# Optimization experiments

Hardware: AMD Instinct MI355X
Metric: run time of the kernel (lower is better)

## Reference

```python
import jax, jax.numpy as jnp
import numpy as np

B, N, E = 2, 20000, 160000
D, U = 1, 100          # input_dim, num_units
IN = D + U             # 101
NEG_SLOPE = 0.2        # PyG GATv2Conv default


def setup_inputs() -> dict:
    key = jax.random.key(0)
    ks = jax.random.split(key, 20)
    s = 0.1
    inp = {
        "inputs": jax.random.normal(ks[0], (B, N * D), jnp.float32),
        "state": jax.random.normal(ks[1], (B, N * U), jnp.float32),
        "src": jax.random.randint(ks[2], (E,), 0, N),
        "dst": jax.random.randint(ks[3], (E,), 0, N),
        # GATv2Conv(101, 200) params: lin_l, lin_r, att, out-bias
        "Wl1": jax.random.normal(ks[4], (IN, 2 * U), jnp.float32) * s,
        "bl1": jax.random.normal(ks[5], (2 * U,), jnp.float32) * s,
        "Wr1": jax.random.normal(ks[6], (IN, 2 * U), jnp.float32) * s,
        "br1": jax.random.normal(ks[7], (2 * U,), jnp.float32) * s,
        "att1": jax.random.normal(ks[8], (2 * U,), jnp.float32) * s,
        "bg1": jax.random.normal(ks[9], (2 * U,), jnp.float32) * s,
        "bias0": jax.random.normal(ks[10], (2 * U,), jnp.float32) * s,
        # GATv2Conv(101, 100) params
        "Wl2": jax.random.normal(ks[11], (IN, U), jnp.float32) * s,
        "bl2": jax.random.normal(ks[12], (U,), jnp.float32) * s,
        "Wr2": jax.random.normal(ks[13], (IN, U), jnp.float32) * s,
        "br2": jax.random.normal(ks[14], (U,), jnp.float32) * s,
        "att2": jax.random.normal(ks[15], (U,), jnp.float32) * s,
        "bg2": jax.random.normal(ks[16], (U,), jnp.float32) * s,
        "bias1": jax.random.normal(ks[17], (U,), jnp.float32) * s,
    }
    return inp


def _gatv2(x, src_f, dst_f, Wl, bl, Wr, br, att, bg):
    # x: (B, N, IN); edges (with self-loops) flow src -> dst.
    xl = x @ Wl + bl                                   # (B, N, C) source transform
    xr = x @ Wr + br                                   # (B, N, C) target transform
    msg = jax.nn.leaky_relu(xl[:, src_f] + xr[:, dst_f], NEG_SLOPE)  # (B, Ef, C)
    e = jnp.einsum('bec,c->be', msg, att)              # (B, Ef) attention logits
    seg_max = jax.vmap(lambda v: jax.ops.segment_max(v, dst_f, num_segments=N))(e)
    ea = jnp.exp(e - seg_max[:, dst_f])
    denom = jax.vmap(lambda v: jax.ops.segment_sum(v, dst_f, num_segments=N))(ea)
    alpha = ea / denom[:, dst_f]                       # per-target softmax
    out = jax.vmap(
        lambda a, xs: jax.ops.segment_sum(a[:, None] * xs, dst_f, num_segments=N)
    )(alpha, xl[:, src_f])                             # (B, N, C)
    return out + bg


def reference(inputs, state, src, dst,
              Wl1, bl1, Wr1, br1, att1, bg1, bias0,
              Wl2, bl2, Wr2, br2, att2, bg2, bias1):
    loops = jnp.arange(N)
    src_f = jnp.concatenate([src, loops])              # PyG adds self-loops
    dst_f = jnp.concatenate([dst, loops])
    inputs3 = inputs.reshape(B, N, D)
    state3 = state.reshape(B, N, U)

    # _gc1: GATv2(101 -> 200) + bias_0, sigmoid gates r, u
    xs = jnp.concatenate([inputs3, state3], axis=2)    # (B, N, 101)
    g1 = _gatv2(xs, src_f, dst_f, Wl1, bl1, Wr1, br1, att1, bg1) + bias0
    val = jax.nn.sigmoid(g1)                           # (B, N, 200)
    r = val[..., :U].reshape(B, N * U)
    u = val[..., U:].reshape(B, N * U)

    # _gc2: GATv2(101 -> 100) on [inputs, r*state] + bias_1, tanh
    xs2 = jnp.concatenate([inputs3, (r * state).reshape(B, N, U)], axis=2)
    c = jnp.tanh(_gatv2(xs2, src_f, dst_f, Wl2, bl2, Wr2, br2, att2, bg2) + bias1)
    c = c.reshape(B, N * U)

    new_state = u * state + (1.0 - u) * c              # (B, N*U)
    return new_state
```

## Files before the change

### kernel.cpp

```cpp
#include <hip/hip_runtime.h>
#include <stdint.h>

typedef __attribute__((ext_vector_type(8))) short short8;
typedef __attribute__((ext_vector_type(4))) short short4v;
typedef __attribute__((ext_vector_type(4))) float f32x4;

static constexpr int BB = 2, NN = 20000, UU = 100;
static constexpr int C1 = 200, C2 = 100;
static constexpr int MT = BB * NN;
static constexpr int MPAD = 40064;
static constexpr float NEG = 0.2f;

__device__ __forceinline__ float b2f(short s) {
  union { uint32_t u; float f; } cv; cv.u = ((uint32_t)(uint16_t)s) << 16; return cv.f;
}
__device__ __forceinline__ short f2b(float x) {
  union { float f; uint32_t u; } cv; cv.f = x;
  uint32_t r = cv.u + 0x7FFFu + ((cv.u >> 16) & 1u);
  return (short)(r >> 16);
}

#define GL2LDS(gsrc, ldst)                                                          \
  __builtin_amdgcn_global_load_lds((const __attribute__((address_space(1))) void*)(gsrc), \
                                   (__attribute__((address_space(3))) void*)(ldst), 16, 0, 0)


__global__ void k_prep(const float* __restrict__ inp, const float* __restrict__ st,
                       const float* __restrict__ Wl1, const float* __restrict__ Wr1,
                       const float* __restrict__ Wl2, const float* __restrict__ Wr2,
                       short* __restrict__ A, short* __restrict__ BT1,
                       short* __restrict__ BT2, int* __restrict__ cursor) {
  int t = blockIdx.x * 256 + threadIdx.x;
  if (t < MT * 16) {
    int r = t >> 4, g = t & 15;
    short8 v;
#pragma unroll
    for (int j = 0; j < 8; ++j) {
      int e = g * 8 + j;
      float x = 0.f;
      if (e == 0) x = inp[r];
      else if (e <= 100) x = st[(size_t)r * 100 + e - 1];
      v[j] = f2b(x);
    }
    *(short8*)(A + (size_t)r * 128 + ((g ^ (r & 7)) << 3)) = v;
  }
  if (t < 512 * 16) {
    int n = t >> 4, g = t & 15;
    short8 v;
#pragma unroll
    for (int j = 0; j < 8; ++j) {
      int k = g * 8 + j;
      float x = 0.f;
      if (k < 101 && n < 400)
        x = (n < 200) ? Wl1[(size_t)k * 200 + n] : Wr1[(size_t)k * 200 + n - 200];
      v[j] = f2b(x);
    }
    *(short8*)(BT1 + (size_t)n * 128 + ((g ^ (n & 7)) << 3)) = v;
  }
  if (t < 256 * 16) {
    int n = t >> 4, g = t & 15;
    short8 v;
#pragma unroll
    for (int j = 0; j < 8; ++j) {
      int k = g * 8 + j;
      int ksrc = (k < 100) ? k + 1 : ((k == 100) ? 0 : -1);
      float x = 0.f;
      if (ksrc >= 0 && n < 200)
        x = (n < 100) ? Wl2[(size_t)ksrc * 100 + n] : Wr2[(size_t)ksrc * 100 + n - 100];
      v[j] = f2b(x);
    }
    *(short8*)(BT2 + (size_t)n * 128 + ((g ^ (n & 7)) << 3)) = v;
  }
  if (t < NN) cursor[t] = 0;
}


__global__ void k_hist(const int* __restrict__ dst, int E, int* __restrict__ hist) {
  int e = blockIdx.x * 256 + threadIdx.x;
  if (e < E) atomicAdd(&hist[dst[e]], 1);
}

__global__ __launch_bounds__(1024) void k_scan(int* __restrict__ histcur,
                                               int* __restrict__ rowptr, int N, int E) {
  __shared__ int part[1024];
  int t = threadIdx.x;
  int CH = (N + 1023) / 1024;
  int beg = t * CH; if (beg > N) beg = N;
  int end = beg + CH; if (end > N) end = N;
  int s = 0;
  for (int i = beg; i < end; ++i) s += histcur[i];
  part[t] = s;
  __syncthreads();
  for (int off = 1; off < 1024; off <<= 1) {
    int v = (t >= off) ? part[t - off] : 0;
    __syncthreads();
    part[t] += v;
    __syncthreads();
  }
  int base = (t == 0) ? 0 : part[t - 1];
  for (int i = beg; i < end; ++i) {
    int h = histcur[i];
    rowptr[i] = base;
    histcur[i] = base;
    base += h;
  }
  if (t == 1023) rowptr[N] = part[1023];
}

__global__ void k_scatter(const int* __restrict__ src, const int* __restrict__ dst, int E,
                          int* __restrict__ cursor, int* __restrict__ col) {
  int e = blockIdx.x * 256 + threadIdx.x;
  if (e < E) {
    int p = atomicAdd(&cursor[dst[e]], 1);
    col[p] = src[e];
  }
}


template<int NOUT, int SPLIT>
__global__ __launch_bounds__(256) void k_gemm(
    const short* __restrict__ A, const short* __restrict__ BT,
    const float* __restrict__ bias_l, const float* __restrict__ bias_r,
    short* __restrict__ X) {
  __shared__ __align__(16) short As[128 * 128];
  __shared__ __align__(16) short Bs[128 * 128];
  int tid = threadIdx.x;
  int m0 = blockIdx.x * 128;
  int n0 = blockIdx.y * 128;
  {
    const short* gA = A + (size_t)m0 * 128;
    const short* gB = BT + (size_t)n0 * 128;
#pragma unroll
    for (int i = 0; i < 8; ++i) {
      GL2LDS(gA + i * 2048 + tid * 8, As + i * 2048 + tid * 8);
      GL2LDS(gB + i * 2048 + tid * 8, Bs + i * 2048 + tid * 8);
    }
  }
  __syncthreads();

  int wv = tid >> 6, lane = tid & 63;
  int m_off = (wv & 1) * 64, n_off = (wv >> 1) * 64;
  int lrow = lane & 15, lk = lane >> 4;
  f32x4 acc[4][4];
#pragma unroll
  for (int i = 0; i < 4; ++i)
#pragma unroll
    for (int j = 0; j < 4; ++j) acc[i][j] = (f32x4){0.f, 0.f, 0.f, 0.f};

#pragma unroll
  for (int kk = 0; kk < 4; ++kk) {
    int g = kk * 4 + lk;
    short8 a[4], b[4];
#pragma unroll
    for (int f = 0; f < 4; ++f) {
      int ra = m_off + f * 16 + lrow;
      a[f] = *(const short8*)(As + ra * 128 + ((g ^ (ra & 7)) << 3));
      int rb = n_off + f * 16 + lrow;
      b[f] = *(const short8*)(Bs + rb * 128 + ((g ^ (rb & 7)) << 3));
    }
#pragma unroll
    for (int i = 0; i < 4; ++i)
#pragma unroll
      for (int j = 0; j < 4; ++j)
        acc[i][j] = __builtin_amdgcn_mfma_f32_16x16x32_bf16(a[i], b[j], acc[i][j], 0, 0, 0);
  }

#pragma unroll
  for (int j = 0; j < 4; ++j) {
    int nc = n0 + n_off + j * 16 + lrow;
    bool nok = nc < NOUT;
    float bv = 0.f;
    int coff = 0;
    if (nok) {
      bv   = (nc < SPLIT) ? bias_l[nc] : bias_r[nc - SPLIT];
      coff = (nc < SPLIT) ? nc : 2 * SPLIT + (nc - SPLIT);
    }
#pragma unroll
    for (int i = 0; i < 4; ++i) {
      int mb = m0 + m_off + i * 16 + lk * 4;
#pragma unroll
      for (int r = 0; r < 4; ++r) {
        int m = mb + r;
        if (nok && m < MT) {
          int b_   = (m >= NN) ? 1 : 0;
          int node = m - b_ * NN;
          X[(size_t)node * (4 * SPLIT) + coff + b_ * SPLIT] = f2b(acc[i][j][r] + bv);
        }
      }
    }
  }
}


__global__ __launch_bounds__(256) void k_agg1(
    const short* __restrict__ X1, const int* __restrict__ rowptr, const int* __restrict__ col,
    const float* __restrict__ att, const float* __restrict__ bgv, const float* __restrict__ bias0,
    const float* __restrict__ st, const float* __restrict__ inp,
    short* __restrict__ A2, float* __restrict__ uu) {
  int w = threadIdx.x >> 6, lane = threadIdx.x & 63;
  int n = blockIdx.x * 4 + w;
  if (n >= NN) return;
  int half = lane >> 5, ll = lane & 31;
  int c0 = (ll < 25 ? ll : 24) * 8;
  int idx = half * NN + n;
  const short* xb = X1 + (size_t)half * 200 + c0;

  float attv[8], xrv[8], num[8];
  {
    f32x4 a0 = (f32x4){0,0,0,0}, a1 = (f32x4){0,0,0,0};
    if (ll < 25) { a0 = *(const f32x4*)(att + c0); a1 = *(const f32x4*)(att + c0 + 4); }
#pragma unroll
    for (int q = 0; q < 4; ++q) { attv[q] = a0[q]; attv[4 + q] = a1[q]; }
    short8 xr8 = *(const short8*)(X1 + (size_t)n * 800 + 400 + half * 200 + c0);
#pragma unroll
    for (int q = 0; q < 8; ++q) xrv[q] = (ll < 25) ? b2f(xr8[q]) : 0.f;
  }
  float denom;
  {
    short8 v = *(const short8*)(xb + (size_t)n * 800);
    float xs[8], e = 0.f;
#pragma unroll
    for (int q = 0; q < 8; ++q) {
      xs[q] = b2f(v[q]);
      float msg = xs[q] + xrv[q];
      msg = (msg > 0.f) ? msg : NEG * msg;
      e = fmaf(msg, attv[q], e);
    }
#pragma unroll
    for (int off = 16; off > 0; off >>= 1) e += __shfl_xor(e, off);
    float pe = __expf(e);
    denom = pe;
#pragma unroll
    for (int q = 0; q < 8; ++q) num[q] = pe * xs[q];
  }

  int beg = rowptr[n], end = rowptr[n + 1];
  for (int bp = beg; bp < end; bp += 64) {
    int cnt = min(end - bp, 64);
    int cv = col[bp + (lane < cnt ? lane : 0)];
    int p = 0;
    for (; p + 4 <= cnt; p += 4) {
      int s0 = __shfl(cv, p), s1 = __shfl(cv, p + 1);
      int s2 = __shfl(cv, p + 2), s3 = __shfl(cv, p + 3);
      short8 v0 = *(const short8*)(xb + (size_t)s0 * 800);
      short8 v1 = *(const short8*)(xb + (size_t)s1 * 800);
      short8 v2 = *(const short8*)(xb + (size_t)s2 * 800);
      short8 v3 = *(const short8*)(xb + (size_t)s3 * 800);
      float xs0[8], xs1[8], xs2[8], xs3[8];
      float e0 = 0.f, e1 = 0.f, e2 = 0.f, e3 = 0.f;
#pragma unroll
      for (int q = 0; q < 8; ++q) {
        float m_;
        xs0[q] = b2f(v0[q]); m_ = xs0[q] + xrv[q]; m_ = (m_ > 0.f) ? m_ : NEG * m_; e0 = fmaf(m_, attv[q], e0);
        xs1[q] = b2f(v1[q]); m_ = xs1[q] + xrv[q]; m_ = (m_ > 0.f) ? m_ : NEG * m_; e1 = fmaf(m_, attv[q], e1);
        xs2[q] = b2f(v2[q]); m_ = xs2[q] + xrv[q]; m_ = (m_ > 0.f) ? m_ : NEG * m_; e2 = fmaf(m_, attv[q], e2);
        xs3[q] = b2f(v3[q]); m_ = xs3[q] + xrv[q]; m_ = (m_ > 0.f) ? m_ : NEG * m_; e3 = fmaf(m_, attv[q], e3);
      }
#pragma unroll
      for (int off = 16; off > 0; off >>= 1) {
        e0 += __shfl_xor(e0, off);
        e1 += __shfl_xor(e1, off);
        e2 += __shfl_xor(e2, off);
        e3 += __shfl_xor(e3, off);
      }
      float pe0 = __expf(e0), pe1 = __expf(e1), pe2 = __expf(e2), pe3 = __expf(e3);
      denom += (pe0 + pe1) + (pe2 + pe3);
#pragma unroll
      for (int q = 0; q < 8; ++q)
        num[q] = fmaf(pe3, xs3[q], fmaf(pe2, xs2[q], fmaf(pe1, xs1[q], fmaf(pe0, xs0[q], num[q]))));
    }
    for (; p < cnt; ++p) {
      int s0 = __shfl(cv, p);
      short8 v0 = *(const short8*)(xb + (size_t)s0 * 800);
      float xs0[8], e0 = 0.f;
#pragma unroll
      for (int q = 0; q < 8; ++q) {
        xs0[q] = b2f(v0[q]);
        float m_ = xs0[q] + xrv[q]; m_ = (m_ > 0.f) ? m_ : NEG * m_;
        e0 = fmaf(m_, attv[q], e0);
      }
#pragma unroll
      for (int off = 16; off > 0; off >>= 1) e0 += __shfl_xor(e0, off);
      float pe0 = __expf(e0);
      denom += pe0;
#pragma unroll
      for (int q = 0; q < 8; ++q) num[q] = fmaf(pe0, xs0[q], num[q]);
    }
  }

  float invd = 1.f / denom;
  if (ll < 25) {
    f32x4 g0 = *(const f32x4*)(bgv + c0),   g1 = *(const f32x4*)(bgv + c0 + 4);
    f32x4 h0 = *(const f32x4*)(bias0 + c0), h1 = *(const f32x4*)(bias0 + c0 + 4);
    float vq[8];
#pragma unroll
    for (int q = 0; q < 4; ++q) {
      float o0 = fmaf(num[q], invd, g0[q] + h0[q]);
      vq[q] = 1.f / (1.f + __expf(-o0));
      float o1 = fmaf(num[4 + q], invd, g1[q] + h1[q]);
      vq[4 + q] = 1.f / (1.f + __expf(-o1));
    }
    size_t sb = (size_t)idx * UU;
    if (ll < 12) {
      f32x4 s0 = *(const f32x4*)(st + sb + c0), s1 = *(const f32x4*)(st + sb + c0 + 4);
      short8 wv;
#pragma unroll
      for (int q = 0; q < 4; ++q) { wv[q] = f2b(vq[q] * s0[q]); wv[4 + q] = f2b(vq[4 + q] * s1[q]); }
      *(short8*)(A2 + (size_t)idx * 128 + ((ll ^ (idx & 7)) << 3)) = wv;
    } else if (ll == 12) {
      f32x4 s0 = *(const f32x4*)(st + sb + 96);
      short8 wv;
#pragma unroll
      for (int q = 0; q < 4; ++q) wv[q] = f2b(vq[q] * s0[q]);
      wv[4] = f2b(inp[idx]); wv[5] = 0; wv[6] = 0; wv[7] = 0;
      *(short8*)(A2 + (size_t)idx * 128 + ((12 ^ (idx & 7)) << 3)) = wv;
      *(f32x4*)(uu + sb) = (f32x4){vq[4], vq[5], vq[6], vq[7]};
    } else {
      int uo = c0 - 100;
      *(f32x4*)(uu + sb + uo)     = (f32x4){vq[0], vq[1], vq[2], vq[3]};
      *(f32x4*)(uu + sb + uo + 4) = (f32x4){vq[4], vq[5], vq[6], vq[7]};
      if (ll < 16) {
        short8 z = (short8){0,0,0,0,0,0,0,0};
        *(short8*)(A2 + (size_t)idx * 128 + ((ll ^ (idx & 7)) << 3)) = z;
      }
    }
  }
}

__global__ __launch_bounds__(256) void k_agg2(
    const short* __restrict__ X2, const int* __restrict__ rowptr, const int* __restrict__ col,
    const float* __restrict__ att, const float* __restrict__ bgv, const float* __restrict__ bias1,
    const float* __restrict__ st, float* __restrict__ out) {
  int w = threadIdx.x >> 6, lane = threadIdx.x & 63;
  int n = blockIdx.x * 4 + w;
  if (n >= NN) return;
  int half = lane >> 5, ll = lane & 31;
  int c0 = (ll < 25 ? ll : 24) * 4;
  int idx = half * NN + n;
  const short* xb = X2 + (size_t)half * 100 + c0;

  float attv[4], xrv[4], num[4];
  {
    f32x4 a0 = (f32x4){0,0,0,0};
    if (ll < 25) a0 = *(const f32x4*)(att + c0);
#pragma unroll
    for (int q = 0; q < 4; ++q) attv[q] = a0[q];
    short4v xr4 = *(const short4v*)(X2 + (size_t)n * 400 + 200 + half * 100 + c0);
#pragma unroll
    for (int q = 0; q < 4; ++q) xrv[q] = (ll < 25) ? b2f(xr4[q]) : 0.f;
  }
  float denom;
  {
    short4v v = *(const short4v*)(xb + (size_t)n * 400);
    float xs[4], e = 0.f;
#pragma unroll
    for (int q = 0; q < 4; ++q) {
      xs[q] = b2f(v[q]);
      float msg = xs[q] + xrv[q];
      msg = (msg > 0.f) ? msg : NEG * msg;
      e = fmaf(msg, attv[q], e);
    }
#pragma unroll
    for (int off = 16; off > 0; off >>= 1) e += __shfl_xor(e, off);
    float pe = __expf(e);
    denom = pe;
#pragma unroll
    for (int q = 0; q < 4; ++q) num[q] = pe * xs[q];
  }

  int beg = rowptr[n], end = rowptr[n + 1];
  for (int bp = beg; bp < end; bp += 64) {
    int cnt = min(end - bp, 64);
    int cv = col[bp + (lane < cnt ? lane : 0)];
    int p = 0;
    for (; p + 4 <= cnt; p += 4) {
      int s0 = __shfl(cv, p), s1 = __shfl(cv, p + 1);
      int s2 = __shfl(cv, p + 2), s3 = __shfl(cv, p + 3);
      short4v v0 = *(const short4v*)(xb + (size_t)s0 * 400);
      short4v v1 = *(const short4v*)(xb + (size_t)s1 * 400);
      short4v v2 = *(const short4v*)(xb + (size_t)s2 * 400);
      short4v v3 = *(const short4v*)(xb + (size_t)s3 * 400);
      float xs0[4], xs1[4], xs2[4], xs3[4];
      float e0 = 0.f, e1 = 0.f, e2 = 0.f, e3 = 0.f;
#pragma unroll
      for (int q = 0; q < 4; ++q) {
        float m_;
        xs0[q] = b2f(v0[q]); m_ = xs0[q] + xrv[q]; m_ = (m_ > 0.f) ? m_ : NEG * m_; e0 = fmaf(m_, attv[q], e0);
        xs1[q] = b2f(v1[q]); m_ = xs1[q] + xrv[q]; m_ = (m_ > 0.f) ? m_ : NEG * m_; e1 = fmaf(m_, attv[q], e1);
        xs2[q] = b2f(v2[q]); m_ = xs2[q] + xrv[q]; m_ = (m_ > 0.f) ? m_ : NEG * m_; e2 = fmaf(m_, attv[q], e2);
        xs3[q] = b2f(v3[q]); m_ = xs3[q] + xrv[q]; m_ = (m_ > 0.f) ? m_ : NEG * m_; e3 = fmaf(m_, attv[q], e3);
      }
#pragma unroll
      for (int off = 16; off > 0; off >>= 1) {
        e0 += __shfl_xor(e0, off);
        e1 += __shfl_xor(e1, off);
        e2 += __shfl_xor(e2, off);
        e3 += __shfl_xor(e3, off);
      }
      float pe0 = __expf(e0), pe1 = __expf(e1), pe2 = __expf(e2), pe3 = __expf(e3);
      denom += (pe0 + pe1) + (pe2 + pe3);
#pragma unroll
      for (int q = 0; q < 4; ++q)
        num[q] = fmaf(pe3, xs3[q], fmaf(pe2, xs2[q], fmaf(pe1, xs1[q], fmaf(pe0, xs0[q], num[q]))));
    }
    for (; p < cnt; ++p) {
      int s0 = __shfl(cv, p);
      short4v v0 = *(const short4v*)(xb + (size_t)s0 * 400);
      float xs0[4], e0 = 0.f;
#pragma unroll
      for (int q = 0; q < 4; ++q) {
        xs0[q] = b2f(v0[q]);
        float m_ = xs0[q] + xrv[q]; m_ = (m_ > 0.f) ? m_ : NEG * m_;
        e0 = fmaf(m_, attv[q], e0);
      }
#pragma unroll
      for (int off = 16; off > 0; off >>= 1) e0 += __shfl_xor(e0, off);
      float pe0 = __expf(e0);
      denom += pe0;
#pragma unroll
      for (int q = 0; q < 4; ++q) num[q] = fmaf(pe0, xs0[q], num[q]);
    }
  }

  float invd = 1.f / denom;
  if (ll < 25) {
    f32x4 g0 = *(const f32x4*)(bgv + c0);
    f32x4 h0 = *(const f32x4*)(bias1 + c0);
    size_t sb = (size_t)idx * UU;
    f32x4 uv = *(const f32x4*)(out + sb + c0);
    f32x4 sv = *(const f32x4*)(st + sb + c0);
    f32x4 res;
#pragma unroll
    for (int q = 0; q < 4; ++q) {
      float o   = fmaf(num[q], invd, g0[q] + h0[q]);
      float cvh = tanhf(o);
      res[q] = uv[q] * sv[q] + (1.f - uv[q]) * cvh;
    }
    *(f32x4*)(out + sb + c0) = res;
  }
}


extern "C" void kernel_launch(void* const* d_in, const int* in_sizes, int n_in,
                              void* d_out, int out_size, void* d_ws, size_t ws_size,
                              hipStream_t stream) {
  const float* inp  = (const float*)d_in[0];
  const float* st   = (const float*)d_in[1];
  const int*   src  = (const int*)d_in[2];
  const int*   dst  = (const int*)d_in[3];
  const float* Wl1  = (const float*)d_in[4];
  const float* bl1  = (const float*)d_in[5];
  const float* Wr1  = (const float*)d_in[6];
  const float* br1  = (const float*)d_in[7];
  const float* att1 = (const float*)d_in[8];
  const float* bg1  = (const float*)d_in[9];
  const float* bias0= (const float*)d_in[10];
  const float* Wl2  = (const float*)d_in[11];
  const float* bl2  = (const float*)d_in[12];
  const float* Wr2  = (const float*)d_in[13];
  const float* br2  = (const float*)d_in[14];
  const float* att2 = (const float*)d_in[15];
  const float* bg2  = (const float*)d_in[16];
  const float* bias1= (const float*)d_in[17];

  const int N = NN;
  const int E = in_sizes[2];

  short* X1  = (short*)d_ws;
  short* X2  = X1;
  short* Aws = X1 + (size_t)NN * 800;
  short* BT1 = Aws + (size_t)MPAD * 128;
  short* BT2 = BT1 + 512 * 128;
  int* rowptr = (int*)(BT2 + 256 * 128);
  int* cursor = rowptr + (N + 1);
  int* col    = cursor + N;

  k_prep<<<(MT * 16 + 255) / 256, 256, 0, stream>>>(inp, st, Wl1, Wr1, Wl2, Wr2,
                                                    Aws, BT1, BT2, cursor);
  k_hist<<<(E + 255) / 256, 256, 0, stream>>>(dst, E, cursor);
  k_scan<<<1, 1024, 0, stream>>>(cursor, rowptr, N, E);
  k_scatter<<<(E + 255) / 256, 256, 0, stream>>>(src, dst, E, cursor, col);

  {
    dim3 g(MPAD / 128, 4);
    k_gemm<400, 200><<<g, 256, 0, stream>>>(Aws, BT1, bl1, br1, X1);
  }
  k_agg1<<<(NN + 3) / 4, 256, 0, stream>>>(X1, rowptr, col, att1, bg1, bias0, st, inp,
                                           Aws, (float*)d_out);
  {
    dim3 g(MPAD / 128, 2);
    k_gemm<200, 100><<<g, 256, 0, stream>>>(Aws, BT2, bl2, br2, X2);
  }
  k_agg2<<<(NN + 3) / 4, 256, 0, stream>>>(X2, rowptr, col, att2, bg2, bias1, st,
                                           (float*)d_out);
}
```

Before: 195.4 us.

## Fuse degree histogram into first GEMM launch and simplify aggregation loops

The edge-degree histogram is folded into the first GEMM launch as extra blocks, so it runs alongside the GEMM tiles and one kernel launch goes away. The GEMM grid becomes 1-D, with tile coordinates derived from blockIdx. In both aggregation kernels, the 32-lane attention-logit reduction now uses DPP row operations plus one cross-row shuffle instead of five shuffles. The neighbor loop is restructured to process two edges per step, with a scalar tail for degrees above 64, which reduces register pressure at the cost of less memory-level parallelism per wave.

```diff
diff --git a/kernel.cpp b/kernel.cpp
--- a/kernel.cpp
+++ b/kernel.cpp
@@ -6,9 +6,9 @@
 typedef __attribute__((ext_vector_type(4))) float f32x4;
 
 static constexpr int BB = 2, NN = 20000, UU = 100;
-static constexpr int C1 = 200, C2 = 100;
 static constexpr int MT = BB * NN;
 static constexpr int MPAD = 40064;
+static constexpr int GB1 = 313;
 static constexpr float NEG = 0.2f;
 
 __device__ __forceinline__ float b2f(short s) {
@@ -18,6 +18,19 @@
   union { float f; uint32_t u; } cv; cv.f = x;
   uint32_t r = cv.u + 0x7FFFu + ((cv.u >> 16) & 1u);
   return (short)(r >> 16);
+}
+
+template<int CTRL>
+__device__ __forceinline__ float dppadd(float x) {
+  int v = __builtin_amdgcn_update_dpp(0, __float_as_int(x), CTRL, 0xF, 0xF, false);
+  return x + __int_as_float(v);
+}
+__device__ __forceinline__ float red32(float x) {
+  x = dppadd<0x121>(x);
+  x = dppadd<0x122>(x);
+  x = dppadd<0x124>(x);
+  x = dppadd<0x128>(x);
+  return x + __shfl_xor(x, 16);
 }
 
 #define GL2LDS(gsrc, ldst)                                                          \
@@ -74,11 +87,6 @@
   if (t < NN) cursor[t] = 0;
 }
 
-
-__global__ void k_hist(const int* __restrict__ dst, int E, int* __restrict__ hist) {
-  int e = blockIdx.x * 256 + threadIdx.x;
-  if (e < E) atomicAdd(&hist[dst[e]], 1);
-}
 
 __global__ __launch_bounds__(1024) void k_scan(int* __restrict__ histcur,
                                                int* __restrict__ rowptr, int N, int E) {
@@ -121,12 +129,18 @@
 __global__ __launch_bounds__(256) void k_gemm(
     const short* __restrict__ A, const short* __restrict__ BT,
     const float* __restrict__ bias_l, const float* __restrict__ bias_r,
-    short* __restrict__ X) {
+    short* __restrict__ X, int nbg,
+    const int* __restrict__ dstE, int E, int* __restrict__ hist) {
   __shared__ __align__(16) short As[128 * 128];
   __shared__ __align__(16) short Bs[128 * 128];
   int tid = threadIdx.x;
-  int m0 = blockIdx.x * 128;
-  int n0 = blockIdx.y * 128;
+  if ((int)blockIdx.x >= nbg) {
+    int e = (blockIdx.x - nbg) * 256 + tid;
+    if (e < E) atomicAdd(&hist[dstE[e]], 1);
+    return;
+  }
+  int m0 = (blockIdx.x % GB1) * 128;
+  int n0 = (blockIdx.x / GB1) * 128;
   {
     const short* gA = A + (size_t)m0 * 128;
     const short* gB = BT + (size_t)n0 * 128;
@@ -191,6 +205,17 @@
   }
 }
 
+
+#define EDGE1(S, NUM, DEN, NCH, STRIDE)                                            \
+  { short8 v_ = *(const short8*)(xb + (size_t)(S) * STRIDE);                       \
+    float e_ = 0.f;                                                                \
+    _Pragma("unroll") for (int q = 0; q < NCH; ++q) {                              \
+      float x_ = b2f(v_[q]); float m_ = x_ + xrv[q];                               \
+      m_ = (m_ > 0.f) ? m_ : NEG * m_; e_ = fmaf(m_, attv[q], e_); }               \
+    e_ = red32(e_);                                                                \
+    float p_ = __expf(e_); DEN += p_;                                              \
+    _Pragma("unroll") for (int q = 0; q < NCH; ++q)                                \
+      NUM[q] = fmaf(p_, b2f(v_[q]), NUM[q]); }
 
 __global__ __launch_bounds__(256) void k_agg1(
     const short* __restrict__ X1, const int* __restrict__ rowptr, const int* __restrict__ col,
@@ -226,8 +251,7 @@
       msg = (msg > 0.f) ? msg : NEG * msg;
       e = fmaf(msg, attv[q], e);
     }
-#pragma unroll
-    for (int off = 16; off > 0; off >>= 1) e += __shfl_xor(e, off);
+    e = red32(e);
     float pe = __expf(e);
     denom = pe;
 #pragma unroll
@@ -235,58 +259,34 @@
   }
 
   int beg = rowptr[n], end = rowptr[n + 1];
-  for (int bp = beg; bp < end; bp += 64) {
-    int cnt = min(end - bp, 64);
-    int cv = col[bp + (lane < cnt ? lane : 0)];
-    int p = 0;
-    for (; p + 4 <= cnt; p += 4) {
-      int s0 = __shfl(cv, p), s1 = __shfl(cv, p + 1);
-      int s2 = __shfl(cv, p + 2), s3 = __shfl(cv, p + 3);
-      short8 v0 = *(const short8*)(xb + (size_t)s0 * 800);
-      short8 v1 = *(const short8*)(xb + (size_t)s1 * 800);
-      short8 v2 = *(const short8*)(xb + (size_t)s2 * 800);
-      short8 v3 = *(const short8*)(xb + (size_t)s3 * 800);
-      float xs0[8], xs1[8], xs2[8], xs3[8];
-      float e0 = 0.f, e1 = 0.f, e2 = 0.f, e3 = 0.f;
-#pragma unroll
-      for (int q = 0; q < 8; ++q) {
-        float m_;
-        xs0[q] = b2f(v0[q]); m_ = xs0[q] + xrv[q]; m_ = (m_ > 0.f) ? m_ : NEG * m_; e0 = fmaf(m_, attv[q], e0);
-        xs1[q] = b2f(v1[q]); m_ = xs1[q] + xrv[q]; m_ = (m_ > 0.f) ? m_ : NEG * m_; e1 = fmaf(m_, attv[q], e1);
-        xs2[q] = b2f(v2[q]); m_ = xs2[q] + xrv[q]; m_ = (m_ > 0.f) ? m_ : NEG * m_; e2 = fmaf(m_, attv[q], e2);
-        xs3[q] = b2f(v3[q]); m_ = xs3[q] + xrv[q]; m_ = (m_ > 0.f) ? m_ : NEG * m_; e3 = fmaf(m_, attv[q], e3);
-      }
-#pragma unroll
-      for (int off = 16; off > 0; off >>= 1) {
-        e0 += __shfl_xor(e0, off);
-        e1 += __shfl_xor(e1, off);
-        e2 += __shfl_xor(e2, off);
-        e3 += __shfl_xor(e3, off);
-      }
-      float pe0 = __expf(e0), pe1 = __expf(e1), pe2 = __expf(e2), pe3 = __expf(e3);
-      denom += (pe0 + pe1) + (pe2 + pe3);
-#pragma unroll
-      for (int q = 0; q < 8; ++q)
-        num[q] = fmaf(pe3, xs3[q], fmaf(pe2, xs2[q], fmaf(pe1, xs1[q], fmaf(pe0, xs0[q], num[q]))));
-    }
-    for (; p < cnt; ++p) {
-      int s0 = __shfl(cv, p);
-      short8 v0 = *(const short8*)(xb + (size_t)s0 * 800);
-      float xs0[8], e0 = 0.f;
-#pragma unroll
-      for (int q = 0; q < 8; ++q) {
-        xs0[q] = b2f(v0[q]);
-        float m_ = xs0[q] + xrv[q]; m_ = (m_ > 0.f) ? m_ : NEG * m_;
-        e0 = fmaf(m_, attv[q], e0);
-      }
-#pragma unroll
-      for (int off = 16; off > 0; off >>= 1) e0 += __shfl_xor(e0, off);
-      float pe0 = __expf(e0);
-      denom += pe0;
-#pragma unroll
-      for (int q = 0; q < 8; ++q) num[q] = fmaf(pe0, xs0[q], num[q]);
-    }
-  }
+  int deg = end - beg;
+  int degc = min(deg, 64);
+  int cv = 0;
+  if (deg > 0) cv = col[beg + (lane < degc ? lane : 0)];
+  int p = 0;
+  for (; p + 2 <= degc; p += 2) {
+    int s0 = __shfl(cv, p), s1 = __shfl(cv, p + 1);
+    short8 v0 = *(const short8*)(xb + (size_t)s0 * 800);
+    short8 v1 = *(const short8*)(xb + (size_t)s1 * 800);
+    float e0 = 0.f, e1 = 0.f;
+#pragma unroll
+    for (int q = 0; q < 8; ++q) {
+      float x, m_;
+      x = b2f(v0[q]); m_ = x + xrv[q]; m_ = (m_ > 0.f) ? m_ : NEG * m_; e0 = fmaf(m_, attv[q], e0);
+      x = b2f(v1[q]); m_ = x + xrv[q]; m_ = (m_ > 0.f) ? m_ : NEG * m_; e1 = fmaf(m_, attv[q], e1);
+    }
+    e0 = red32(e0); e1 = red32(e1);
+    float pe0 = __expf(e0), pe1 = __expf(e1);
+    denom += pe0 + pe1;
+#pragma unroll
+    for (int q = 0; q < 8; ++q)
+      num[q] = fmaf(pe1, b2f(v1[q]), fmaf(pe0, b2f(v0[q]), num[q]));
+  }
+  if (p < degc) {
+    int s0 = __shfl(cv, p);
+    EDGE1(s0, num, denom, 8, 800);
+  }
+  for (int t = 64; t < deg; ++t) { int s = col[beg + t]; EDGE1(s, num, denom, 8, 800); }
 
   float invd = 1.f / denom;
   if (ll < 25) {
@@ -360,8 +360,7 @@
       msg = (msg > 0.f) ? msg : NEG * msg;
       e = fmaf(msg, attv[q], e);
     }
-#pragma unroll
-    for (int off = 16; off > 0; off >>= 1) e += __shfl_xor(e, off);
+    e = red32(e);
     float pe = __expf(e);
     denom = pe;
 #pragma unroll
@@ -369,56 +368,57 @@
   }
 
   int beg = rowptr[n], end = rowptr[n + 1];
-  for (int bp = beg; bp < end; bp += 64) {
-    int cnt = min(end - bp, 64);
-    int cv = col[bp + (lane < cnt ? lane : 0)];
-    int p = 0;
-    for (; p + 4 <= cnt; p += 4) {
-      int s0 = __shfl(cv, p), s1 = __shfl(cv, p + 1);
-      int s2 = __shfl(cv, p + 2), s3 = __shfl(cv, p + 3);
-      short4v v0 = *(const short4v*)(xb + (size_t)s0 * 400);
-      short4v v1 = *(const short4v*)(xb + (size_t)s1 * 400);
-      short4v v2 = *(const short4v*)(xb + (size_t)s2 * 400);
-      short4v v3 = *(const short4v*)(xb + (size_t)s3 * 400);
-      float xs0[4], xs1[4], xs2[4], xs3[4];
-      float e0 = 0.f, e1 = 0.f, e2 = 0.f, e3 = 0.f;
+  int deg = end - beg;
+  int degc = min(deg, 64);
+  int cv = 0;
+  if (deg > 0) cv = col[beg + (lane < degc ? lane : 0)];
+  int p = 0;
+  for (; p + 2 <= degc; p += 2) {
+    int s0 = __shfl(cv, p), s1 = __shfl(cv, p + 1);
+    short4v v0 = *(const short4v*)(xb + (size_t)s0 * 400);
+    short4v v1 = *(const short4v*)(xb + (size_t)s1 * 400);
+    float e0 = 0.f, e1 = 0.f;
+#pragma unroll
+    for (int q = 0; q < 4; ++q) {
+      float x, m_;
+      x = b2f(v0[q]); m_ = x + xrv[q]; m_ = (m_ > 0.f) ? m_ : NEG * m_; e0 = fmaf(m_, attv[q], e0);
+      x = b2f(v1[q]); m_ = x + xrv[q]; m_ = (m_ > 0.f) ? m_ : NEG * m_; e1 = fmaf(m_, attv[q], e1);
+    }
+    e0 = red32(e0); e1 = red32(e1);
+    float pe0 = __expf(e0), pe1 = __expf(e1);
+    denom += pe0 + pe1;
+#pragma unroll
+    for (int q = 0; q < 4; ++q)
+      num[q] = fmaf(pe1, b2f(v1[q]), fmaf(pe0, b2f(v0[q]), num[q]));
+  }
+  if (p < degc) {
+    int s0 = __shfl(cv, p);
+    { short4v v_ = *(const short4v*)(xb + (size_t)s0 * 400);
+      float e_ = 0.f;
 #pragma unroll
       for (int q = 0; q < 4; ++q) {
-        float m_;
-        xs0[q] = b2f(v0[q]); m_ = xs0[q] + xrv[q]; m_ = (m_ > 0.f) ? m_ : NEG * m_; e0 = fmaf(m_, attv[q], e0);
-        xs1[q] = b2f(v1[q]); m_ = xs1[q] + xrv[q]; m_ = (m_ > 0.f) ? m_ : NEG * m_; e1 = fmaf(m_, attv[q], e1);
-        xs2[q] = b2f(v2[q]); m_ = xs2[q] + xrv[q]; m_ = (m_ > 0.f) ? m_ : NEG * m_; e2 = fmaf(m_, attv[q], e2);
-        xs3[q] = b2f(v3[q]); m_ = xs3[q] + xrv[q]; m_ = (m_ > 0.f) ? m_ : NEG * m_; e3 = fmaf(m_, attv[q], e3);
+        float x_ = b2f(v_[q]); float m_ = x_ + xrv[q];
+        m_ = (m_ > 0.f) ? m_ : NEG * m_; e_ = fmaf(m_, attv[q], e_);
       }
-#pragma unroll
-      for (int off = 16; off > 0; off >>= 1) {
-        e0 += __shfl_xor(e0, off);
-        e1 += __shfl_xor(e1, off);
-        e2 += __shfl_xor(e2, off);
-        e3 += __shfl_xor(e3, off);
+      e_ = red32(e_);
+      float p_ = __expf(e_); denom += p_;
+#pragma unroll
+      for (int q = 0; q < 4; ++q) num[q] = fmaf(p_, b2f(v_[q]), num[q]);
+    }
+  }
+  for (int t = 64; t < deg; ++t) {
+    int s = col[beg + t];
+    { short4v v_ = *(const short4v*)(xb + (size_t)s * 400);
+      float e_ = 0.f;
+#pragma unroll
+      for (int q = 0; q < 4; ++q) {
+        float x_ = b2f(v_[q]); float m_ = x_ + xrv[q];
+        m_ = (m_ > 0.f) ? m_ : NEG * m_; e_ = fmaf(m_, attv[q], e_);
       }
-      float pe0 = __expf(e0), pe1 = __expf(e1), pe2 = __expf(e2), pe3 = __expf(e3);
-      denom += (pe0 + pe1) + (pe2 + pe3);
-#pragma unroll
-      for (int q = 0; q < 4; ++q)
-        num[q] = fmaf(pe3, xs3[q], fmaf(pe2, xs2[q], fmaf(pe1, xs1[q], fmaf(pe0, xs0[q], num[q]))));
-    }
-    for (; p < cnt; ++p) {
-      int s0 = __shfl(cv, p);
-      short4v v0 = *(const short4v*)(xb + (size_t)s0 * 400);
-      float xs0[4], e0 = 0.f;
-#pragma unroll
-      for (int q = 0; q < 4; ++q) {
-        xs0[q] = b2f(v0[q]);
-        float m_ = xs0[q] + xrv[q]; m_ = (m_ > 0.f) ? m_ : NEG * m_;
-        e0 = fmaf(m_, attv[q], e0);
-      }
-#pragma unroll
-      for (int off = 16; off > 0; off >>= 1) e0 += __shfl_xor(e0, off);
-      float pe0 = __expf(e0);
-      denom += pe0;
-#pragma unroll
-      for (int q = 0; q < 4; ++q) num[q] = fmaf(pe0, xs0[q], num[q]);
+      e_ = red32(e_);
+      float p_ = __expf(e_); denom += p_;
+#pragma unroll
+      for (int q = 0; q < 4; ++q) num[q] = fmaf(p_, b2f(v_[q]), num[q]);
     }
   }
 
@@ -477,20 +477,18 @@
 
   k_prep<<<(MT * 16 + 255) / 256, 256, 0, stream>>>(inp, st, Wl1, Wr1, Wl2, Wr2,
                                                     Aws, BT1, BT2, cursor);
-  k_hist<<<(E + 255) / 256, 256, 0, stream>>>(dst, E, cursor);
+  {
+    int nbg = GB1 * 4;
+    int nbh = (E + 255) / 256;
+    k_gemm<400, 200><<<nbg + nbh, 256, 0, stream>>>(Aws, BT1, bl1, br1, X1, nbg,
+                                                    dst, E, cursor);
+  }
   k_scan<<<1, 1024, 0, stream>>>(cursor, rowptr, N, E);
   k_scatter<<<(E + 255) / 256, 256, 0, stream>>>(src, dst, E, cursor, col);
-
-  {
-    dim3 g(MPAD / 128, 4);
-    k_gemm<400, 200><<<g, 256, 0, stream>>>(Aws, BT1, bl1, br1, X1);
-  }
   k_agg1<<<(NN + 3) / 4, 256, 0, stream>>>(X1, rowptr, col, att1, bg1, bias0, st, inp,
                                            Aws, (float*)d_out);
-  {
-    dim3 g(MPAD / 128, 2);
-    k_gemm<200, 100><<<g, 256, 0, stream>>>(Aws, BT2, bl2, br2, X2);
-  }
+  k_gemm<200, 100><<<GB1 * 2, 256, 0, stream>>>(Aws, BT2, bl2, br2, X2, GB1 * 2,
+                                                nullptr, 0, nullptr);
   k_agg2<<<(NN + 3) / 4, 256, 0, stream>>>(X2, rowptr, col, att2, bg2, bias1, st,
                                            (float*)d_out);
 }
```

Result: faster. 180.6 us (-7.6%).
